# Optimization experiments

Hardware: AMD Instinct MI355X
Metric: run time of the kernel (lower is better)

## Reference

```python
import jax, jax.numpy as jnp
import numpy as np

EPS = 1e-5

def _ln(x, g, b):
    m = jnp.mean(x, axis=-1, keepdims=True)
    v = jnp.mean((x - m) ** 2, axis=-1, keepdims=True)
    return (x - m) * jax.lax.rsqrt(v + EPS) * g + b


def setup_inputs() -> dict:
    key = jax.random.key(0)
    B, T, C, H, A = 4, 1024, 1024, 16, 64
    ks = jax.random.split(key, 16)
    s = 0.02
    inp = {
        "x": jax.random.normal(ks[0], (B, T, C), jnp.float32),
        "ln1_g": jnp.ones((C,), jnp.float32), "ln1_b": jnp.zeros((C,), jnp.float32),
        "ln2_g": jnp.ones((C,), jnp.float32), "ln2_b": jnp.zeros((C,), jnp.float32),
        "ln3_g": jnp.ones((C,), jnp.float32), "ln3_b": jnp.zeros((C,), jnp.float32),
        "wq": jax.random.normal(ks[1], (C, C), jnp.float32) * s, "bq": jnp.zeros((C,), jnp.float32),
        "wk": jax.random.normal(ks[2], (C, C), jnp.float32) * s, "bk": jnp.zeros((C,), jnp.float32),
        "wv": jax.random.normal(ks[3], (C, C), jnp.float32) * s, "bv": jnp.zeros((C,), jnp.float32),
        "wo": jax.random.normal(ks[4], (C, C), jnp.float32) * s, "bo": jnp.zeros((C,), jnp.float32),
        "w1": jax.random.normal(ks[5], (C, 4 * C), jnp.float32) * s, "b1": jnp.zeros((4 * C,), jnp.float32),
        "w2": jax.random.normal(ks[6], (4 * C, C), jnp.float32) * s, "b2": jnp.zeros((C,), jnp.float32),
        "wd": jax.random.normal(ks[7], (C, A), jnp.float32) * 1e-4, "bd": jnp.zeros((A,), jnp.float32),
        "wu": jax.random.normal(ks[8], (A, C), jnp.float32) * 1e-4, "bu": jnp.zeros((C,), jnp.float32),
    }
    return inp


def _block(x, ln1_g, ln1_b, ln2_g, ln2_b, ln3_g, ln3_b,
           wq, bq, wk, bk, wv, bv, wo, bo, w1, b1, w2, b2, wd, bd, wu, bu):
    B, T, C = x.shape
    H = 16
    D = C // H
    normed = _ln(x, ln3_g, ln3_b)  # ln3 of original input, used by adapter

    # --- causal self-attention on ln1(x) ---
    h = _ln(x, ln1_g, ln1_b)
    q = (h @ wq + bq).reshape(B, T, H, D)
    k = (h @ wk + bk).reshape(B, T, H, D)
    v = (h @ wv + bv).reshape(B, T, H, D)
    att = jnp.einsum('bqhd,bkhd->bhqk', q, k) * (1.0 / np.sqrt(D))
    causal = jnp.tril(jnp.ones((T, T), bool))
    att = jnp.where(causal, att, -jnp.inf)
    att = jax.nn.softmax(att, axis=-1)
    y = jnp.einsum('bhqk,bkhd->bqhd', att, v).reshape(B, T, C)
    attn_out = y @ wo + bo

    hidden = x + attn_out
    # --- MLP on ln2(hidden) ---
    m = _ln(hidden, ln2_g, ln2_b)
    mlp_out = jax.nn.gelu(m @ w1 + b1, approximate=False) @ w2 + b2
    forward_states = hidden + mlp_out

    # --- adapter on ln3(original x) ---
    a = jax.nn.relu(normed @ wd + bd) @ wu + bu

    # dropout is identity (p=0 / eval)
    return hidden + forward_states + a


def reference(x, ln1_g, ln1_b, ln2_g, ln2_b, ln3_g, ln3_b,
              wq, bq, wk, bk, wv, bv, wo, bo, w1, b1, w2, b2, wd, bd, wu, bu):
    return _block(x, ln1_g, ln1_b, ln2_g, ln2_b, ln3_g, ln3_b,
                  wq, bq, wk, bk, wv, bv, wo, bo, w1, b1, w2, b2, wd, bd, wu, bu)
```

## Files before the change

kernel.cpp:

```cpp
#include <hip/hip_runtime.h>

typedef unsigned short u16;
typedef __bf16 bf16x8 __attribute__((ext_vector_type(8)));
typedef u16    u16x8  __attribute__((ext_vector_type(8)));
typedef float  f32x4  __attribute__((ext_vector_type(4)));

__device__ __forceinline__ u16 f2bf(float f) {
    union { float f; unsigned u; } x{f};
    unsigned r = x.u + 0x7fffu + ((x.u >> 16) & 1u);
    return (u16)(r >> 16);
}
__device__ __forceinline__ float bf2f(u16 h) {
    union { unsigned u; float f; } x{(unsigned)h << 16};
    return x.f;
}

__device__ __forceinline__ f32x4 mfma16(bf16x8 a, bf16x8 b, f32x4 c) {
    return __builtin_amdgcn_mfma_f32_16x16x32_bf16(a, b, c, 0, 0, 0);
}

__device__ __forceinline__ void async_ld16(const void* g, void* l) {
    __builtin_amdgcn_global_load_lds(
        (const __attribute__((address_space(1))) unsigned int*)g,
        (__attribute__((address_space(3))) unsigned int*)l, 16, 0, 0);
}

struct PrepParams {
    const float* src[8];
    u16* dst[8];
    int K[8], N[8];
    int pfx[9];
    const float *bq, *bk, *bv;
    float* bqkv;
};

__global__ void prep_kernel(PrepParams p) {
    const int b = blockIdx.x;
    if (b >= p.pfx[8]) {
        int i = (b - p.pfx[8]) * 256 + threadIdx.x;
        p.bqkv[i] = i < 1024 ? p.bq[i] : (i < 2048 ? p.bk[i - 1024] : p.bv[i - 2048]);
        return;
    }
    int j = 0;
    while (b >= p.pfx[j + 1]) ++j;
    const float* __restrict__ in = p.src[j];
    u16* __restrict__ out = p.dst[j];
    const int K = p.K[j], N = p.N[j];
    const int local = b - p.pfx[j];
    const int tx = N >> 6;
    const int n0 = (local % tx) * 64, k0 = (local / tx) * 64;

    __shared__ float tile[64][65];
    const int tid = threadIdx.x;
    const int rr = tid >> 4, cc = tid & 15;
#pragma unroll
    for (int it = 0; it < 4; ++it) {
        const int r = rr + it * 16;
        float4 v = *(const float4*)(in + (long)(k0 + r) * N + n0 + cc * 4);
        tile[r][cc * 4 + 0] = v.x; tile[r][cc * 4 + 1] = v.y;
        tile[r][cc * 4 + 2] = v.z; tile[r][cc * 4 + 3] = v.w;
    }
    __syncthreads();
#pragma unroll
    for (int it = 0; it < 4; ++it) {
        const int n = rr + it * 16;
        ushort4 o;
        o.x = f2bf(tile[cc * 4 + 0][n]);
        o.y = f2bf(tile[cc * 4 + 1][n]);
        o.z = f2bf(tile[cc * 4 + 2][n]);
        o.w = f2bf(tile[cc * 4 + 3][n]);
        *(ushort4*)(out + (long)(n0 + n) * K + k0 + cc * 4) = o;
    }
}

__global__ void ln_dual_kernel(const float* __restrict__ x,
                               const float* __restrict__ g1, const float* __restrict__ b1,
                               const float* __restrict__ g3, const float* __restrict__ b3,
                               u16* __restrict__ out1, u16* __restrict__ out3) {
    const int row = blockIdx.x;
    const long base = (long)row * 1024;
    const int t = threadIdx.x;
    float4 v = ((const float4*)(x + base))[t];
    float s = v.x + v.y + v.z + v.w;
    float ss = v.x * v.x + v.y * v.y + v.z * v.z + v.w * v.w;
    for (int o = 32; o > 0; o >>= 1) { s += __shfl_down(s, o); ss += __shfl_down(ss, o); }
    __shared__ float red[8];
    if ((t & 63) == 0) { red[t >> 6] = s; red[(t >> 6) + 4] = ss; }
    __syncthreads();
    float sum = red[0] + red[1] + red[2] + red[3];
    float sq  = red[4] + red[5] + red[6] + red[7];
    const float mean = sum * (1.f / 1024.f);
    const float rstd = rsqrtf(sq * (1.f / 1024.f) - mean * mean + 1e-5f);
    float4 G1 = ((const float4*)g1)[t], B1 = ((const float4*)b1)[t];
    float4 G3 = ((const float4*)g3)[t], B3 = ((const float4*)b3)[t];
    float n0 = (v.x - mean) * rstd, n1 = (v.y - mean) * rstd;
    float n2 = (v.z - mean) * rstd, n3 = (v.w - mean) * rstd;
    ushort4 o1, o3;
    o1.x = f2bf(n0 * G1.x + B1.x); o1.y = f2bf(n1 * G1.y + B1.y);
    o1.z = f2bf(n2 * G1.z + B1.z); o1.w = f2bf(n3 * G1.w + B1.w);
    o3.x = f2bf(n0 * G3.x + B3.x); o3.y = f2bf(n1 * G3.y + B3.y);
    o3.z = f2bf(n2 * G3.z + B3.z); o3.w = f2bf(n3 * G3.w + B3.w);
    ((ushort4*)(out1 + base))[t] = o1;
    ((ushort4*)(out3 + base))[t] = o3;
}

__global__ void ln_single_kernel(const float* __restrict__ x,
                                 const float* __restrict__ g, const float* __restrict__ b,
                                 u16* __restrict__ out) {
    const int row = blockIdx.x;
    const long base = (long)row * 1024;
    const int t = threadIdx.x;
    float4 v = ((const float4*)(x + base))[t];
    float s = v.x + v.y + v.z + v.w;
    float ss = v.x * v.x + v.y * v.y + v.z * v.z + v.w * v.w;
    for (int o = 32; o > 0; o >>= 1) { s += __shfl_down(s, o); ss += __shfl_down(ss, o); }
    __shared__ float red[8];
    if ((t & 63) == 0) { red[t >> 6] = s; red[(t >> 6) + 4] = ss; }
    __syncthreads();
    float sum = red[0] + red[1] + red[2] + red[3];
    float sq  = red[4] + red[5] + red[6] + red[7];
    const float mean = sum * (1.f / 1024.f);
    const float rstd = rsqrtf(sq * (1.f / 1024.f) - mean * mean + 1e-5f);
    float4 G = ((const float4*)g)[t], B = ((const float4*)b)[t];
    ushort4 o;
    o.x = f2bf((v.x - mean) * rstd * G.x + B.x);
    o.y = f2bf((v.y - mean) * rstd * G.y + B.y);
    o.z = f2bf((v.z - mean) * rstd * G.z + B.z);
    o.w = f2bf((v.w - mean) * rstd * G.w + B.w);
    ((ushort4*)(out + base))[t] = o;
}

__global__ void transpose_v(const u16* __restrict__ qkv, u16* __restrict__ vT) {
    const int bh = blockIdx.z, b = bh >> 4, hh = bh & 15;
    const int t0 = blockIdx.x * 32, d0 = blockIdx.y * 32;
    __shared__ u16 tile[32][33];
    const u16* src = qkv + (long)(b * 1024) * 3072 + 2048 + hh * 64;
    for (int i = threadIdx.y; i < 32; i += 8)
        tile[i][threadIdx.x] = src[(long)(t0 + i) * 3072 + d0 + threadIdx.x];
    __syncthreads();
    u16* dst = vT + (long)bh * 64 * 1024;
    for (int i = threadIdx.y; i < 32; i += 8)
        dst[(long)(d0 + i) * 1024 + t0 + threadIdx.x] = tile[threadIdx.x][i];
}

__global__ void reduce_out4(float* __restrict__ out, const u16* __restrict__ p,
                            const float* __restrict__ b2) {
    const long base = (long)blockIdx.x * 1024;
    const int t = threadIdx.x;
    float4 sum = {0.f, 0.f, 0.f, 0.f};
#pragma unroll
    for (int z = 0; z < 4; ++z) {
        ushort4 q = ((const ushort4*)(p + (long)z * (4096L * 1024) + base))[t];
        sum.x += bf2f(q.x); sum.y += bf2f(q.y);
        sum.z += bf2f(q.z); sum.w += bf2f(q.w);
    }
    float4 bias = ((const float4*)b2)[t];
    float4 o = ((const float4*)(out + base))[t];
    o.x += sum.x + bias.x; o.y += sum.y + bias.y;
    o.z += sum.z + bias.z; o.w += sum.w + bias.w;
    ((float4*)(out + base))[t] = o;
}

template <int BN, typename Epi>
__global__ __launch_bounds__(256, 4)
void gemm_kernel(const u16* __restrict__ A, const u16* __restrict__ Bt,
                 int M, int N, int K, int ld, Epi epi) {
    constexpr int AE = 128 * 32;
    constexpr int BE = BN * 32;
    constexpr int MI = (BN == 128) ? 4 : 2;
    __shared__ u16 sm[2][AE + BE];
    const int tid = threadIdx.x;
    const int m0 = blockIdx.y * 128;
    const int n0 = blockIdx.x * BN;
    const int k0g = blockIdx.z * K;
    const int wid = tid >> 6, lane = tid & 63;
    const int lr = lane & 15, lh = lane >> 4;
    const int wm = (BN == 128) ? (wid >> 1) * 64 : wid * 32;
    const int wn = (BN == 128) ? (wid & 1) * 64 : 0;

    const int cr = lane >> 2, lq = lane & 3;
    const int ra0 = wid * 32 + cr, ra1 = ra0 + 16;
    const int qa0 = lq ^ (ra0 & 3) ^ ((ra0 >> 2) & 3);
    const int qa1 = lq ^ (ra1 & 3) ^ ((ra1 >> 2) & 3);
    const long aoff0 = (long)(m0 + ra0) * ld + k0g + qa0 * 8;
    const long aoff1 = (long)(m0 + ra1) * ld + k0g + qa1 * 8;
    const int la0 = wid * 1024, la1 = la0 + 512;

    long boff0, boff1 = 0;
    int lb0, lb1 = 0;
    if (BN == 128) {
        boff0 = (long)min(n0 + ra0, N - 1) * ld + k0g + qa0 * 8;
        boff1 = (long)min(n0 + ra1, N - 1) * ld + k0g + qa1 * 8;
        lb0 = AE + wid * 1024; lb1 = lb0 + 512;
    } else {
        const int rb = wid * 16 + cr;
        const int qb = lq ^ (rb & 3) ^ ((rb >> 2) & 3);
        boff0 = (long)min(n0 + rb, N - 1) * ld + k0g + qb * 8;
        lb0 = AE + wid * 512;
    }

    const int qoff = ((lh ^ (lr & 3) ^ ((lr >> 2) & 3)) & 3) * 8;

    f32x4 acc[MI][4] = {};
    const int nk = K / 32;

    auto stage = [&](int kt) {
        const long ko = (long)kt * 32;
        u16* s = sm[kt & 1];
        async_ld16(A + aoff0 + ko, s + la0);
        async_ld16(A + aoff1 + ko, s + la1);
        async_ld16(Bt + boff0 + ko, s + lb0);
        if constexpr (BN == 128) async_ld16(Bt + boff1 + ko, s + lb1);
    };
    auto compute = [&](int kt) {
        const u16* sA = sm[kt & 1];
        const u16* sB = sA + AE;
        bf16x8 af[MI], bfr[4];
#pragma unroll
        for (int i = 0; i < MI; ++i)
            af[i] = *(const bf16x8*)(sA + (wm + i * 16 + lr) * 32 + qoff);
#pragma unroll
        for (int j = 0; j < 4; ++j)
            bfr[j] = *(const bf16x8*)(sB + (wn + j * 16 + lr) * 32 + qoff);
#pragma unroll
        for (int i = 0; i < MI; ++i)
#pragma unroll
            for (int j = 0; j < 4; ++j)
                acc[i][j] = mfma16(af[i], bfr[j], acc[i][j]);
    };

    stage(0);
    __syncthreads();
    for (int kt = 0; kt < nk; ++kt) {
        if (kt + 1 < nk) stage(kt + 1);
        compute(kt);
        __syncthreads();
    }

#pragma unroll
    for (int i = 0; i < MI; ++i)
#pragma unroll
        for (int j = 0; j < 4; ++j) {
            const int col = n0 + wn + j * 16 + lr;
            if (col < N) {
#pragma unroll
                for (int r = 0; r < 4; ++r) {
                    const int row = m0 + wm + i * 16 + lh * 4 + r;
                    epi(row, col, acc[i][j][r]);
                }
            }
        }
}

struct EpiBF16Bias {
    u16* out; const float* bias; int ldo;
    __device__ void operator()(int r, int c, float v) const {
        out[(long)r * ldo + c] = f2bf(v + bias[c]);
    }
};
struct EpiResid {
    float* hidden; const float* bias; const float* x;
    __device__ void operator()(int r, int c, float v) const {
        long i = (long)r * 1024 + c; hidden[i] = v + bias[c] + x[i];
    }
};
struct EpiGelu {
    u16* out; const float* bias;
    __device__ void operator()(int r, int c, float v) const {
        float x = v + bias[c];
        float u2 = x * (1.5957691216f + 0.0713548162726f * x * x);
        float g = x / (1.f + __expf(-u2));
        out[(long)r * 4096 + c] = f2bf(g);
    }
};
struct EpiReluBF16 {
    u16* out; const float* bias;
    __device__ void operator()(int r, int c, float v) const {
        out[(long)r * 64 + c] = f2bf(fmaxf(v + bias[c], 0.f));
    }
};
struct EpiAdapter {
    float* out; const float* bias; const float* hidden;
    __device__ void operator()(int r, int c, float v) const {
        long i = (long)r * 1024 + c; out[i] = 2.f * hidden[i] + v + bias[c];
    }
};
struct EpiStoreSplit {
    u16* p;
    __device__ void operator()(int r, int c, float v) const {
        p[(long)blockIdx.z * (4096L * 1024) + (long)r * 1024 + c] = f2bf(v);
    }
};

__global__ __launch_bounds__(256, 2)
void attn_kernel(const u16* __restrict__ qkv, const u16* __restrict__ vT,
                 u16* __restrict__ y) {
    const int bh = blockIdx.x, b = bh >> 4, hh = bh & 15;
    const int q0 = blockIdx.y * 128;
    const int tid = threadIdx.x, wid = tid >> 6, lane = tid & 63;
    const int lr = lane & 15, lh = lane >> 4;
    const int qw = q0 + wid * 32;

    __shared__ u16 smK[64 * 72];
    __shared__ u16 smV[64 * 72];
    __shared__ u16 smP[4 * 32 * 72];
    u16* pw = smP + wid * (32 * 72);

    const u16* qbase = qkv + (long)(b * 1024) * 3072 + hh * 64;
    const u16* kbase = qbase + 1024;
    const u16* vbase = vT + (long)bh * 64 * 1024;

    bf16x8 a_q[2][2];
#pragma unroll
    for (int mt = 0; mt < 2; ++mt)
#pragma unroll
        for (int ks = 0; ks < 2; ++ks) {
            uint4 t = *(const uint4*)(qbase + (long)(qw + mt * 16 + lr) * 3072 + ks * 32 + lh * 8);
            a_q[mt][ks] = __builtin_bit_cast(bf16x8, t);
        }

    bf16x8 ones;
    { u16x8 t = {0x3F80, 0x3F80, 0x3F80, 0x3F80, 0x3F80, 0x3F80, 0x3F80, 0x3F80};
      ones = __builtin_bit_cast(bf16x8, t); }

    f32x4 o_acc[2][4] = {};
    f32x4 l_acc[2] = {};
    f32x4 m_run[2] = {{-1e30f, -1e30f, -1e30f, -1e30f}, {-1e30f, -1e30f, -1e30f, -1e30f}};

    const int ntiles = q0 / 64 + 2;
    const int ck = tid >> 3, cs = (tid & 7) * 8;
    const int ck2 = (tid + 256) >> 3, cs2 = ((tid + 256) & 7) * 8;
    for (int kt = 0; kt < ntiles; ++kt) {
        const int k0 = kt * 64;
        __syncthreads();
        {
            uint4 kv0 = *(const uint4*)(kbase + (long)(k0 + ck) * 3072 + cs);
            uint4 kv1 = *(const uint4*)(kbase + (long)(k0 + ck2) * 3072 + cs2);
            *(uint4*)(smK + ck * 72 + cs) = kv0;
            *(uint4*)(smK + ck2 * 72 + cs2) = kv1;
            uint4 vv0 = *(const uint4*)(vbase + (long)ck * 1024 + k0 + cs);
            uint4 vv1 = *(const uint4*)(vbase + (long)ck2 * 1024 + k0 + cs2);
            *(uint4*)(smV + ck * 72 + cs) = vv0;
            *(uint4*)(smV + ck2 * 72 + cs2) = vv1;
        }
        __syncthreads();
        if (k0 > qw + 31) continue;

        bf16x8 bK[4][2];
#pragma unroll
        for (int nt = 0; nt < 4; ++nt)
#pragma unroll
            for (int ks = 0; ks < 2; ++ks)
                bK[nt][ks] = *(const bf16x8*)(smK + (nt * 16 + lr) * 72 + ks * 32 + lh * 8);

        f32x4 s[2][4];
#pragma unroll
        for (int mt = 0; mt < 2; ++mt)
#pragma unroll
            for (int nt = 0; nt < 4; ++nt) {
                f32x4 z = {0.f, 0.f, 0.f, 0.f};
                z = mfma16(a_q[mt][0], bK[nt][0], z);
                z = mfma16(a_q[mt][1], bK[nt][1], z);
                s[mt][nt] = z;
            }
#pragma unroll
        for (int mt = 0; mt < 2; ++mt) {
            const int qb = qw + mt * 16 + lh * 4;
#pragma unroll
            for (int nt = 0; nt < 4; ++nt) {
                const int kkg = k0 + nt * 16 + lr;
#pragma unroll
                for (int r = 0; r < 4; ++r) {
                    float v = s[mt][nt][r] * 0.125f;
                    if (kkg > qb + r) v = -1e30f;
                    s[mt][nt][r] = v;
                }
            }
        }
#pragma unroll
        for (int mt = 0; mt < 2; ++mt) {
            f32x4 mx = s[mt][0];
#pragma unroll
            for (int nt = 1; nt < 4; ++nt)
#pragma unroll
                for (int r = 0; r < 4; ++r) mx[r] = fmaxf(mx[r], s[mt][nt][r]);
#pragma unroll
            for (int xm = 1; xm < 16; xm <<= 1)
#pragma unroll
                for (int r = 0; r < 4; ++r) mx[r] = fmaxf(mx[r], __shfl_xor(mx[r], xm));
            f32x4 mnew, alpha;
#pragma unroll
            for (int r = 0; r < 4; ++r) {
                mnew[r] = fmaxf(m_run[mt][r], mx[r]);
                alpha[r] = __expf(m_run[mt][r] - mnew[r]);
            }
            m_run[mt] = mnew;
            l_acc[mt] *= alpha;
#pragma unroll
            for (int dt = 0; dt < 4; ++dt) o_acc[mt][dt] *= alpha;
#pragma unroll
            for (int nt = 0; nt < 4; ++nt)
#pragma unroll
                for (int r = 0; r < 4; ++r)
                    s[mt][nt][r] = __expf(s[mt][nt][r] - mnew[r]);
#pragma unroll
            for (int nt = 0; nt < 4; ++nt)
#pragma unroll
                for (int r = 0; r < 4; ++r)
                    pw[(mt * 16 + lh * 4 + r) * 72 + nt * 16 + lr] = f2bf(s[mt][nt][r]);
        }
        bf16x8 vf[4][2];
#pragma unroll
        for (int dt = 0; dt < 4; ++dt)
#pragma unroll
            for (int ks = 0; ks < 2; ++ks)
                vf[dt][ks] = *(const bf16x8*)(smV + (dt * 16 + lr) * 72 + ks * 32 + lh * 8);
#pragma unroll
        for (int mt = 0; mt < 2; ++mt) {
            bf16x8 pf0 = *(const bf16x8*)(pw + (mt * 16 + lr) * 72 + lh * 8);
            bf16x8 pf1 = *(const bf16x8*)(pw + (mt * 16 + lr) * 72 + 32 + lh * 8);
            l_acc[mt] = mfma16(pf0, ones, l_acc[mt]);
            l_acc[mt] = mfma16(pf1, ones, l_acc[mt]);
#pragma unroll
            for (int dt = 0; dt < 4; ++dt) {
                o_acc[mt][dt] = mfma16(pf0, vf[dt][0], o_acc[mt][dt]);
                o_acc[mt][dt] = mfma16(pf1, vf[dt][1], o_acc[mt][dt]);
            }
        }
    }
#pragma unroll
    for (int mt = 0; mt < 2; ++mt) {
        f32x4 linv;
#pragma unroll
        for (int r = 0; r < 4; ++r) linv[r] = 1.f / l_acc[mt][r];
#pragma unroll
        for (int dt = 0; dt < 4; ++dt) {
#pragma unroll
            for (int r = 0; r < 4; ++r) {
                const int tok = b * 1024 + qw + mt * 16 + lh * 4 + r;
                y[(long)tok * 1024 + hh * 64 + dt * 16 + lr] = f2bf(o_acc[mt][dt][r] * linv[r]);
            }
        }
    }
}

extern "C" void kernel_launch(void* const* d_in, const int* in_sizes, int n_in,
                              void* d_out, int out_size, void* d_ws, size_t ws_size,
                              hipStream_t stream) {
    const float* x    = (const float*)d_in[0];
    const float* ln1g = (const float*)d_in[1];
    const float* ln1b = (const float*)d_in[2];
    const float* ln2g = (const float*)d_in[3];
    const float* ln2b = (const float*)d_in[4];
    const float* ln3g = (const float*)d_in[5];
    const float* ln3b = (const float*)d_in[6];
    const float* wq = (const float*)d_in[7];  const float* bq = (const float*)d_in[8];
    const float* wk = (const float*)d_in[9];  const float* bk = (const float*)d_in[10];
    const float* wv = (const float*)d_in[11]; const float* bv = (const float*)d_in[12];
    const float* wo = (const float*)d_in[13]; const float* bo = (const float*)d_in[14];
    const float* w1 = (const float*)d_in[15]; const float* b1 = (const float*)d_in[16];
    const float* w2 = (const float*)d_in[17]; const float* b2 = (const float*)d_in[18];
    const float* wd = (const float*)d_in[19]; const float* bd = (const float*)d_in[20];
    const float* wu = (const float*)d_in[21]; const float* bu = (const float*)d_in[22];
    float* out = (float*)d_out;

    char* base = (char*)d_ws;
    size_t off = 0;
    auto carve = [&](size_t bytes) -> char* {
        char* p = base + off; off += (bytes + 255) & ~(size_t)255; return p;
    };
    u16* qkv_wt = (u16*)carve(3072L * 1024 * 2);
    u16* wo_t   = (u16*)carve(1024L * 1024 * 2);
    u16* w1_t   = (u16*)carve(4096L * 1024 * 2);
    u16* w2_t   = (u16*)carve(1024L * 4096 * 2);
    u16* wd_t   = (u16*)carve(64L * 1024 * 2);
    u16* wu_t   = (u16*)carve(1024L * 64 * 2);
    float* bqkv = (float*)carve(3072L * 4);
    u16* hbuf   = (u16*)carve(4096L * 1024 * 2);
    u16* nrm    = (u16*)carve(4096L * 1024 * 2);
    u16* qkvb   = (u16*)carve(4096L * 3072 * 2);
    u16* vT     = (u16*)carve(64L * 64 * 1024 * 2);
    u16* ybuf   = (u16*)carve(4096L * 1024 * 2);
    float* hid  = (float*)carve(4096L * 1024 * 4);
    u16* mbuf   = (u16*)carve(4096L * 1024 * 2);
    u16* act    = (u16*)carve(4096L * 4096 * 2);
    u16* t1     = (u16*)carve(4096L * 64 * 2);
    u16* part   = (u16*)carve(4L * 4096 * 1024 * 2);

    PrepParams pp;
    pp.src[0] = wq; pp.dst[0] = qkv_wt;                 pp.K[0] = 1024; pp.N[0] = 1024;
    pp.src[1] = wk; pp.dst[1] = qkv_wt + 1024L * 1024;  pp.K[1] = 1024; pp.N[1] = 1024;
    pp.src[2] = wv; pp.dst[2] = qkv_wt + 2048L * 1024;  pp.K[2] = 1024; pp.N[2] = 1024;
    pp.src[3] = wo; pp.dst[3] = wo_t;                   pp.K[3] = 1024; pp.N[3] = 1024;
    pp.src[4] = w1; pp.dst[4] = w1_t;                   pp.K[4] = 1024; pp.N[4] = 4096;
    pp.src[5] = w2; pp.dst[5] = w2_t;                   pp.K[5] = 4096; pp.N[5] = 1024;
    pp.src[6] = wd; pp.dst[6] = wd_t;                   pp.K[6] = 1024; pp.N[6] = 64;
    pp.src[7] = wu; pp.dst[7] = wu_t;                   pp.K[7] = 64;   pp.N[7] = 1024;
    int acc_blocks = 0;
    for (int j = 0; j < 8; ++j) {
        pp.pfx[j] = acc_blocks;
        acc_blocks += (pp.N[j] >> 6) * (pp.K[j] >> 6);
    }
    pp.pfx[8] = acc_blocks;
    pp.bq = bq; pp.bk = bk; pp.bv = bv; pp.bqkv = bqkv;
    prep_kernel<<<acc_blocks + 12, 256, 0, stream>>>(pp);

    ln_dual_kernel<<<4096, 256, 0, stream>>>(x, ln1g, ln1b, ln3g, ln3b, hbuf, nrm);

    gemm_kernel<128><<<dim3(24, 32), 256, 0, stream>>>(hbuf, qkv_wt, 4096, 3072, 1024, 1024,
                                                       EpiBF16Bias{qkvb, bqkv, 3072});
    transpose_v<<<dim3(32, 2, 64), dim3(32, 8), 0, stream>>>(qkvb, vT);
    attn_kernel<<<dim3(64, 8), 256, 0, stream>>>(qkvb, vT, ybuf);
    gemm_kernel<64><<<dim3(16, 32), 256, 0, stream>>>(ybuf, wo_t, 4096, 1024, 1024, 1024,
                                                      EpiResid{hid, bo, x});
    ln_single_kernel<<<4096, 256, 0, stream>>>(hid, ln2g, ln2b, mbuf);
    gemm_kernel<128><<<dim3(32, 32), 256, 0, stream>>>(mbuf, w1_t, 4096, 4096, 1024, 1024,
                                                       EpiGelu{act, b1});
    gemm_kernel<64><<<dim3(1, 32), 256, 0, stream>>>(nrm, wd_t, 4096, 64, 1024, 1024,
                                                     EpiReluBF16{t1, bd});
    gemm_kernel<64><<<dim3(16, 32), 256, 0, stream>>>(t1, wu_t, 4096, 1024, 64, 64,
                                                      EpiAdapter{out, bu, hid});
    gemm_kernel<128><<<dim3(8, 32, 4), 256, 0, stream>>>(act, w2_t, 4096, 1024, 1024, 4096,
                                                         EpiStoreSplit{part});
    reduce_out4<<<4096, 256, 0, stream>>>(out, part, b2);
}
```

Baseline: 411.5 us.

## Replace LDS-tiled GEMM with single-wave register-direct 64x64 GEMM

Replaces the 256-thread shared-memory GEMM, which used async global-to-LDS loads and double buffering, with a 64-thread kernel. The new kernel loads MFMA fragments directly from global memory into registers and double-buffers them in registers. This removes the LDS staging and block-wide barriers, and it launches more, smaller blocks. The cost is that operand reuse across waves through shared memory is lost, which raises global/L2 traffic, and the loads are strided, less coalesced 16-byte rows.

```diff
diff --git a/kernel.cpp b/kernel.cpp
--- a/kernel.cpp
+++ b/kernel.cpp
@@ -17,12 +17,6 @@
 
 __device__ __forceinline__ f32x4 mfma16(bf16x8 a, bf16x8 b, f32x4 c) {
     return __builtin_amdgcn_mfma_f32_16x16x32_bf16(a, b, c, 0, 0, 0);
-}
-
-__device__ __forceinline__ void async_ld16(const void* g, void* l) {
-    __builtin_amdgcn_global_load_lds(
-        (const __attribute__((address_space(1))) unsigned int*)g,
-        (__attribute__((address_space(3))) unsigned int*)l, 16, 0, 0);
 }
 
 struct PrepParams {
@@ -161,94 +155,58 @@
     ((float4*)(out + base))[t] = o;
 }
 
-template <int BN, typename Epi>
-__global__ __launch_bounds__(256, 4)
-void gemm_kernel(const u16* __restrict__ A, const u16* __restrict__ Bt,
-                 int M, int N, int K, int ld, Epi epi) {
-    constexpr int AE = 128 * 32;
-    constexpr int BE = BN * 32;
-    constexpr int MI = (BN == 128) ? 4 : 2;
-    __shared__ u16 sm[2][AE + BE];
-    const int tid = threadIdx.x;
-    const int m0 = blockIdx.y * 128;
-    const int n0 = blockIdx.x * BN;
-    const int k0g = blockIdx.z * K;
-    const int wid = tid >> 6, lane = tid & 63;
+template <typename Epi>
+__global__ __launch_bounds__(64)
+void gemm_rr(const u16* __restrict__ A, const u16* __restrict__ Bt,
+             int K, int ld, Epi epi) {
+    const int lane = threadIdx.x;
     const int lr = lane & 15, lh = lane >> 4;
-    const int wm = (BN == 128) ? (wid >> 1) * 64 : wid * 32;
-    const int wn = (BN == 128) ? (wid & 1) * 64 : 0;
-
-    const int cr = lane >> 2, lq = lane & 3;
-    const int ra0 = wid * 32 + cr, ra1 = ra0 + 16;
-    const int qa0 = lq ^ (ra0 & 3) ^ ((ra0 >> 2) & 3);
-    const int qa1 = lq ^ (ra1 & 3) ^ ((ra1 >> 2) & 3);
-    const long aoff0 = (long)(m0 + ra0) * ld + k0g + qa0 * 8;
-    const long aoff1 = (long)(m0 + ra1) * ld + k0g + qa1 * 8;
-    const int la0 = wid * 1024, la1 = la0 + 512;
-
-    long boff0, boff1 = 0;
-    int lb0, lb1 = 0;
-    if (BN == 128) {
-        boff0 = (long)min(n0 + ra0, N - 1) * ld + k0g + qa0 * 8;
-        boff1 = (long)min(n0 + ra1, N - 1) * ld + k0g + qa1 * 8;
-        lb0 = AE + wid * 1024; lb1 = lb0 + 512;
-    } else {
-        const int rb = wid * 16 + cr;
-        const int qb = lq ^ (rb & 3) ^ ((rb >> 2) & 3);
-        boff0 = (long)min(n0 + rb, N - 1) * ld + k0g + qb * 8;
-        lb0 = AE + wid * 512;
-    }
-
-    const int qoff = ((lh ^ (lr & 3) ^ ((lr >> 2) & 3)) & 3) * 8;
-
-    f32x4 acc[MI][4] = {};
+    const int m0 = blockIdx.y * 64, n0 = blockIdx.x * 64;
+    const long k0g = (long)blockIdx.z * K;
+    const u16* Ab = A + (long)m0 * ld + k0g + lh * 8;
+    const u16* Bb = Bt + (long)n0 * ld + k0g + lh * 8;
+
+    f32x4 acc[4][4] = {};
+    bf16x8 a0[4], b0[4], a1[4], b1[4];
     const int nk = K / 32;
 
-    auto stage = [&](int kt) {
+    auto ld_tile = [&](bf16x8* af, bf16x8* bf_, int kt) {
         const long ko = (long)kt * 32;
-        u16* s = sm[kt & 1];
-        async_ld16(A + aoff0 + ko, s + la0);
-        async_ld16(A + aoff1 + ko, s + la1);
-        async_ld16(Bt + boff0 + ko, s + lb0);
-        if constexpr (BN == 128) async_ld16(Bt + boff1 + ko, s + lb1);
+#pragma unroll
+        for (int i = 0; i < 4; ++i)
+            af[i] = *(const bf16x8*)(Ab + (long)(i * 16 + lr) * ld + ko);
+#pragma unroll
+        for (int j = 0; j < 4; ++j)
+            bf_[j] = *(const bf16x8*)(Bb + (long)(j * 16 + lr) * ld + ko);
     };
-    auto compute = [&](int kt) {
-        const u16* sA = sm[kt & 1];
-        const u16* sB = sA + AE;
-        bf16x8 af[MI], bfr[4];
-#pragma unroll
-        for (int i = 0; i < MI; ++i)
-            af[i] = *(const bf16x8*)(sA + (wm + i * 16 + lr) * 32 + qoff);
-#pragma unroll
-        for (int j = 0; j < 4; ++j)
-            bfr[j] = *(const bf16x8*)(sB + (wn + j * 16 + lr) * 32 + qoff);
-#pragma unroll
-        for (int i = 0; i < MI; ++i)
+    auto do_mfma = [&](bf16x8* af, bf16x8* bf_) {
+#pragma unroll
+        for (int i = 0; i < 4; ++i)
 #pragma unroll
             for (int j = 0; j < 4; ++j)
-                acc[i][j] = mfma16(af[i], bfr[j], acc[i][j]);
+                acc[i][j] = mfma16(af[i], bf_[j], acc[i][j]);
     };
 
-    stage(0);
-    __syncthreads();
-    for (int kt = 0; kt < nk; ++kt) {
-        if (kt + 1 < nk) stage(kt + 1);
-        compute(kt);
-        __syncthreads();
-    }
-
-#pragma unroll
-    for (int i = 0; i < MI; ++i)
+    ld_tile(a0, b0, 0);
+    int kt = 0;
+    for (; kt + 2 < nk; kt += 2) {
+        ld_tile(a1, b1, kt + 1);
+        do_mfma(a0, b0);
+        ld_tile(a0, b0, kt + 2);
+        do_mfma(a1, b1);
+    }
+    ld_tile(a1, b1, kt + 1);
+    do_mfma(a0, b0);
+    do_mfma(a1, b1);
+
+#pragma unroll
+    for (int i = 0; i < 4; ++i)
 #pragma unroll
         for (int j = 0; j < 4; ++j) {
-            const int col = n0 + wn + j * 16 + lr;
-            if (col < N) {
-#pragma unroll
-                for (int r = 0; r < 4; ++r) {
-                    const int row = m0 + wm + i * 16 + lh * 4 + r;
-                    epi(row, col, acc[i][j][r]);
-                }
-            }
+            const int col = n0 + j * 16 + lr;
+#pragma unroll
+            for (int r = 0; r < 4; ++r)
+                epi(m0 + i * 16 + lh * 4 + r, col, acc[i][j][r]);
         }
 }
 
@@ -507,20 +465,20 @@
 
     ln_dual_kernel<<<4096, 256, 0, stream>>>(x, ln1g, ln1b, ln3g, ln3b, hbuf, nrm);
 
-    gemm_kernel<128><<<dim3(24, 32), 256, 0, stream>>>(hbuf, qkv_wt, 4096, 3072, 1024, 1024,
-                                                       EpiBF16Bias{qkvb, bqkv, 3072});
+    gemm_rr<<<dim3(48, 64), 64, 0, stream>>>(hbuf, qkv_wt, 1024, 1024,
+                                             EpiBF16Bias{qkvb, bqkv, 3072});
     transpose_v<<<dim3(32, 2, 64), dim3(32, 8), 0, stream>>>(qkvb, vT);
     attn_kernel<<<dim3(64, 8), 256, 0, stream>>>(qkvb, vT, ybuf);
-    gemm_kernel<64><<<dim3(16, 32), 256, 0, stream>>>(ybuf, wo_t, 4096, 1024, 1024, 1024,
-                                                      EpiResid{hid, bo, x});
+    gemm_rr<<<dim3(16, 64), 64, 0, stream>>>(ybuf, wo_t, 1024, 1024,
+                                             EpiResid{hid, bo, x});
     ln_single_kernel<<<4096, 256, 0, stream>>>(hid, ln2g, ln2b, mbuf);
-    gemm_kernel<128><<<dim3(32, 32), 256, 0, stream>>>(mbuf, w1_t, 4096, 4096, 1024, 1024,
-                                                       EpiGelu{act, b1});
-    gemm_kernel<64><<<dim3(1, 32), 256, 0, stream>>>(nrm, wd_t, 4096, 64, 1024, 1024,
-                                                     EpiReluBF16{t1, bd});
-    gemm_kernel<64><<<dim3(16, 32), 256, 0, stream>>>(t1, wu_t, 4096, 1024, 64, 64,
-                                                      EpiAdapter{out, bu, hid});
-    gemm_kernel<128><<<dim3(8, 32, 4), 256, 0, stream>>>(act, w2_t, 4096, 1024, 1024, 4096,
-                                                         EpiStoreSplit{part});
+    gemm_rr<<<dim3(64, 64), 64, 0, stream>>>(mbuf, w1_t, 1024, 1024,
+                                             EpiGelu{act, b1});
+    gemm_rr<<<dim3(1, 64), 64, 0, stream>>>(nrm, wd_t, 1024, 1024,
+                                            EpiReluBF16{t1, bd});
+    gemm_rr<<<dim3(16, 64), 64, 0, stream>>>(t1, wu_t, 64, 64,
+                                             EpiAdapter{out, bu, hid});
+    gemm_rr<<<dim3(16, 64, 4), 64, 0, stream>>>(act, w2_t, 1024, 4096,
+                                                EpiStoreSplit{part});
     reduce_out4<<<4096, 256, 0, stream>>>(out, part, b2);
 }
```

Result: slower. 637.8 us (+55.0%).
